# Performance work log

Hardware: AMD Instinct MI355X
Metric: run time of the kernel (lower is better)

## Reference

```python
import jax, jax.numpy as jnp
import numpy as np

B = 4096          # players (batch)
DEG = 64          # asteroids per player
A = B * DEG       # total asteroids
E = A             # one edge per asteroid (asteroid -> its player)
PD, AD, ED = 5, 3, 7
HID = 64
HEADS = 4
OUT = HID         # GATv2Conv out_channels (concat=False -> mean over heads)
L = 2             # num_layers
NEG_SLOPE = 0.2
LN_EPS = 1e-5


def setup_inputs() -> dict:
    key = jax.random.key(0)
    ks = jax.random.split(key, 20)
    f = jnp.float32
    inp = {}
    inp["player_feat"] = jax.random.normal(ks[0], (B, PD), f)
    inp["asteroid_feat"] = jax.random.normal(ks[1], (A, AD), f)
    src = jnp.arange(E, dtype=jnp.int32)
    dst = src // DEG                      # player batch index per edge
    inp["edge_index"] = jnp.stack([src, dst])  # [2, E] int32
    inp["edge_attr"] = jax.random.normal(ks[2], (E, ED), f)
    sc = 0.1
    # input projections
    inp["Wp"] = jax.random.normal(ks[3], (PD, HID), f) * sc
    inp["bp"] = jnp.zeros((HID,), f)
    inp["Wa"] = jax.random.normal(ks[4], (AD, HID), f) * sc
    inp["ba"] = jnp.zeros((HID,), f)
    # per-layer GATv2 params (stacked over L)
    inp["Wl"] = jax.random.normal(ks[5], (L, HID, HEADS * OUT), f) * sc
    inp["bl"] = jnp.zeros((L, HEADS * OUT), f)
    inp["Wr"] = jax.random.normal(ks[6], (L, HID, HEADS * OUT), f) * sc
    inp["br"] = jnp.zeros((L, HEADS * OUT), f)
    inp["We"] = jax.random.normal(ks[7], (L, ED, HEADS * OUT), f) * sc
    inp["att"] = jax.random.normal(ks[8], (L, HEADS, OUT), f) * sc
    inp["bias"] = jnp.zeros((L, OUT), f)
    inp["ln_g"] = jnp.ones((L, HID), f)
    inp["ln_b"] = jnp.zeros((L, HID), f)
    return inp


def _layer_norm(x, g, b):
    mu = jnp.mean(x, axis=-1, keepdims=True)
    var = jnp.mean(jnp.square(x - mu), axis=-1, keepdims=True)
    return (x - mu) * jax.lax.rsqrt(var + LN_EPS) * g + b


def _gatv2(x, src, dst, edge_attr, Wl, bl, Wr, br, We, att, bias, n_nodes):
    # x: [N, HID]; src/dst: [E]; PyG GATv2Conv, add_self_loops=False, concat=False
    xl = (x @ Wl + bl).reshape(-1, HEADS, OUT)   # source transform
    xr = (x @ Wr + br).reshape(-1, HEADS, OUT)   # target transform
    ea = (edge_attr @ We).reshape(-1, HEADS, OUT)
    e = xl[src] + xr[dst] + ea                   # [E, H, O]
    e = jnp.where(e >= 0, e, NEG_SLOPE * e)      # LeakyReLU(0.2)
    logits = jnp.einsum('eho,ho->eh', e, att)    # [E, H]
    # segment softmax over incoming edges of each target node
    m = jax.ops.segment_max(logits, dst, num_segments=n_nodes)
    al = jnp.exp(logits - m[dst])
    den = jax.ops.segment_sum(al, dst, num_segments=n_nodes)
    alpha = al / den[dst]                        # [E, H]
    msg = alpha[:, :, None] * xl[src]            # [E, H, O]
    out = jax.ops.segment_sum(msg, dst, num_segments=n_nodes)  # [N, H, O]
    return jnp.mean(out, axis=1) + bias          # concat=False -> head mean


def reference(player_feat, asteroid_feat, edge_index, edge_attr,
              Wp, bp, Wa, ba, Wl, bl, Wr, br, We, att, bias, ln_g, ln_b):
    batch = player_feat.shape[0]
    h_p = jax.nn.relu(player_feat @ Wp + bp)
    h_a = jax.nn.relu(asteroid_feat @ Wa + ba)
    x = jnp.concatenate([h_p, h_a], axis=0)      # [N, HID]
    n_nodes = x.shape[0]
    src = edge_index[0] + batch                  # asteroid local -> global idx
    dst = edge_index[1]
    for i in range(L):
        x_new = _gatv2(x, src, dst, edge_attr, Wl[i], bl[i], Wr[i], br[i],
                       We[i], att[i], bias[i], n_nodes)
        x = _layer_norm(x + jax.nn.relu(x_new), ln_g[i], ln_b[i])
    return x[:batch]
```

## Files before the change

### kernel.cpp

```cpp
#include <hip/hip_runtime.h>


typedef __bf16 bf16x8 __attribute__((ext_vector_type(8)));
typedef float  f32x4  __attribute__((ext_vector_type(4)));

union FragU { unsigned short u[8]; bf16x8 v; };

__device__ __forceinline__ float bf2f(unsigned short u) {
    union { unsigned int i; float f; } v; v.i = ((unsigned int)u) << 16; return v.f;
}
__device__ __forceinline__ unsigned short f2bf(float f) {
    union { float f; unsigned int i; } v; v.f = f;
    unsigned int r = v.i + 0x7fffu + ((v.i >> 16) & 1u);
    return (unsigned short)(r >> 16);
}

#define NEG_SLOPE 0.2f
#define LN_EPS 1e-5f
#define XS 88

struct Smem {
    __align__(16) unsigned short xa[64 * XS];
    float xp[64];
    float xr[256];
    float outp[256];
    float afs[192];
    float rbs[64], gs[64], bs[64];
};

__global__ __launch_bounds__(256) void prep_weights(
    const float* __restrict__ Wl, const float* __restrict__ We,
    unsigned short* __restrict__ wlf, unsigned short* __restrict__ wef)
{
    int i = blockIdx.x * 256 + threadIdx.x;
    {
        int jj = i & 7, t = (i >> 3) & 255, frag = (i >> 11) & 7, layer = (i >> 14) & 1;
        int nt = frag >> 1, ko = frag & 1;
        int c = (t >> 6) * 64 + nt * 16 + (t & 15);
        int kb = ko * 32 + ((t >> 4) & 3) * 8;
        wlf[i] = f2bf(Wl[layer * 16384 + (kb + jj) * 256 + c]);
    }
    if (i < 16384) {
        int jj = i & 7, t = (i >> 3) & 255, nt = (i >> 11) & 3, layer = (i >> 13) & 1;
        int q = (t >> 4) & 3;
        int c = (t >> 6) * 64 + nt * 16 + (t & 15);
        wef[i] = (q == 0 && jj < 7) ? f2bf(We[layer * 1792 + jj * 256 + c])
                                    : (unsigned short)0;
    }
}

template <bool WS>
__global__ __launch_bounds__(256) void gnn_main(
    const float* __restrict__ pf, const float* __restrict__ af,
    const float* __restrict__ eat, const float* __restrict__ Wp,
    const float* __restrict__ bp, const float* __restrict__ Wa,
    const float* __restrict__ ba, const float* __restrict__ Wl,
    const float* __restrict__ bl, const float* __restrict__ Wr,
    const float* __restrict__ br, const float* __restrict__ We,
    const float* __restrict__ att, const float* __restrict__ bias,
    const float* __restrict__ lng, const float* __restrict__ lnb,
    const unsigned short* __restrict__ wlf, const unsigned short* __restrict__ wef,
    float* __restrict__ out)
{
    __shared__ Smem sm;
    const int p = blockIdx.x, t = threadIdx.x;
    const int w = t >> 6, l = t & 63, q = l >> 4, m = l & 15;
    const int cbase = w * 64;

    if (t < 192) sm.afs[t] = af[p * 192 + t];
    if (t < 64) {
        sm.rbs[t] = fmaxf(bias[t], 0.f);
        sm.gs[t] = lng[t];
        sm.bs[t] = lnb[t];
        float acc = bp[t];
        #pragma unroll
        for (int d = 0; d < 5; ++d) acc += pf[p * 5 + d] * Wp[d * 64 + t];
        sm.xp[t] = fmaxf(acc, 0.f);
    }
    __syncthreads();
    {
        const int k = t & 63;
        float wa0 = Wa[k], wa1 = Wa[64 + k], wa2 = Wa[128 + k], bak = ba[k];
        #pragma unroll
        for (int rep = 0; rep < 16; ++rep) {
            int j = rep * 4 + (t >> 6);
            float acc = bak + sm.afs[j * 3] * wa0 + sm.afs[j * 3 + 1] * wa1
                      + sm.afs[j * 3 + 2] * wa2;
            sm.xa[j * XS + k] = f2bf(fmaxf(acc, 0.f));
        }
    }
    #pragma unroll
    for (int idx = t; idx < 512; idx += 256) {
        int j = idx >> 3, d = idx & 7;
        sm.xa[j * XS + 64 + d] = (d < 7) ? f2bf(eat[(p * 64 + j) * 7 + d])
                                         : (unsigned short)0;
    }
    __syncthreads();

    f32x4 accT[16];

    for (int layer = 0; layer < 2; ++layer) {
        {
            float acc = br[layer * 256 + t];
            const float* Wri = Wr + layer * 16384 + t;
            #pragma unroll 16
            for (int k = 0; k < 64; ++k) acc += sm.xp[k] * Wri[k * 256];
            sm.xr[t] = acc;
        }
        __syncthreads();

        FragU bfr[8];
        bf16x8 ebf[4];
        if constexpr (WS) {
            #pragma unroll
            for (int f = 0; f < 8; ++f)
                bfr[f].v = *reinterpret_cast<const bf16x8*>(&wlf[((layer * 8 + f) * 256 + t) * 8]);
            #pragma unroll
            for (int nt = 0; nt < 4; ++nt)
                ebf[nt] = *reinterpret_cast<const bf16x8*>(&wef[((layer * 4 + nt) * 256 + t) * 8]);
        } else {
            const float* Wli = Wl + layer * 16384;
            #pragma unroll
            for (int nt = 0; nt < 4; ++nt) {
                int c = cbase + nt * 16 + m;
                #pragma unroll
                for (int ko = 0; ko < 2; ++ko) {
                    int kb = ko * 32 + q * 8;
                    #pragma unroll
                    for (int jj = 0; jj < 8; ++jj)
                        bfr[nt * 2 + ko].u[jj] = f2bf(Wli[(kb + jj) * 256 + c]);
                }
                FragU e;
                #pragma unroll
                for (int jj = 0; jj < 8; ++jj)
                    e.u[jj] = (q == 0 && jj < 7) ? f2bf(We[layer * 1792 + jj * 256 + c])
                                                 : (unsigned short)0;
                ebf[nt] = e.v;
            }
        }
        float blc[4], xrc[4], aoc[4];
        #pragma unroll
        for (int nt = 0; nt < 4; ++nt) {
            int c = cbase + nt * 16 + m;
            blc[nt] = bl[layer * 256 + c];
            aoc[nt] = att[layer * 256 + c];
            xrc[nt] = sm.xr[c];
        }

        float lp[16];
        #pragma unroll
        for (int i = 0; i < 16; ++i) lp[i] = 0.f;

        #pragma unroll
        for (int mt = 0; mt < 4; ++mt) {
            const int row = mt * 16 + m;
            bf16x8 a0 = *reinterpret_cast<const bf16x8*>(&sm.xa[row * XS + q * 8]);
            bf16x8 a1 = *reinterpret_cast<const bf16x8*>(&sm.xa[row * XS + 32 + q * 8]);
            bf16x8 a2 = *reinterpret_cast<const bf16x8*>(&sm.xa[row * XS + 64]);
            #pragma unroll
            for (int nt = 0; nt < 4; ++nt) {
                f32x4 c1 = { blc[nt], blc[nt], blc[nt], blc[nt] };
                c1 = __builtin_amdgcn_mfma_f32_16x16x32_bf16(a0, bfr[nt * 2 + 0].v, c1, 0, 0, 0);
                c1 = __builtin_amdgcn_mfma_f32_16x16x32_bf16(a1, bfr[nt * 2 + 1].v, c1, 0, 0, 0);
                accT[mt * 4 + nt] = c1;
                f32x4 c2 = { xrc[nt], xrc[nt], xrc[nt], xrc[nt] };
                c2 = __builtin_amdgcn_mfma_f32_16x16x32_bf16(a2, ebf[nt], c2, 0, 0, 0);
                #pragma unroll
                for (int r = 0; r < 4; ++r) {
                    float ev = c1[r] + c2[r];
                    ev = (ev >= 0.f) ? ev : NEG_SLOPE * ev;
                    lp[mt * 4 + r] += ev * aoc[nt];
                }
            }
        }

        #pragma unroll
        for (int i = 0; i < 16; ++i) {
            float v = lp[i];
            v += __shfl_xor(v, 1, 64);
            v += __shfl_xor(v, 2, 64);
            v += __shfl_xor(v, 4, 64);
            v += __shfl_xor(v, 8, 64);
            lp[i] = v;
        }
        float mx = lp[0];
        #pragma unroll
        for (int i = 1; i < 16; ++i) mx = fmaxf(mx, lp[i]);
        mx = fmaxf(mx, __shfl_xor(mx, 16, 64));
        mx = fmaxf(mx, __shfl_xor(mx, 32, 64));
        float den = 0.f;
        #pragma unroll
        for (int i = 0; i < 16; ++i) { lp[i] = __expf(lp[i] - mx); den += lp[i]; }
        den += __shfl_xor(den, 16, 64);
        den += __shfl_xor(den, 32, 64);
        const float rden = 1.f / den;

        #pragma unroll
        for (int nt = 0; nt < 4; ++nt) {
            float s = 0.f;
            #pragma unroll
            for (int mt = 0; mt < 4; ++mt) {
                f32x4 c = accT[mt * 4 + nt];
                #pragma unroll
                for (int r = 0; r < 4; ++r) s += lp[mt * 4 + r] * c[r];
            }
            s *= rden;
            s += __shfl_xor(s, 16, 64);
            s += __shfl_xor(s, 32, 64);
            if (q == 0) sm.outp[cbase + nt * 16 + m] = s;
        }
        __syncthreads();

        if (layer == 0) {
            const int j = t >> 2, part = t & 3;
            unsigned short* rowp = &sm.xa[j * XS + part * 16];
            FragU A0, A1;
            A0.v = *reinterpret_cast<const bf16x8*>(rowp);
            A1.v = *reinterpret_cast<const bf16x8*>(rowp + 8);
            float v[16], sum = 0.f, sq = 0.f;
            #pragma unroll
            for (int i = 0; i < 16; ++i) {
                unsigned short us = (i < 8) ? A0.u[i] : A1.u[i - 8];
                float x = bf2f(us) + sm.rbs[part * 16 + i];
                v[i] = x; sum += x; sq += x * x;
            }
            sum += __shfl_xor(sum, 1, 64); sq += __shfl_xor(sq, 1, 64);
            sum += __shfl_xor(sum, 2, 64); sq += __shfl_xor(sq, 2, 64);
            float mu = sum * (1.f / 64.f);
            float var = sq * (1.f / 64.f) - mu * mu;
            float rs = rsqrtf(var + LN_EPS);
            FragU O0, O1;
            #pragma unroll
            for (int i = 0; i < 16; ++i) {
                int col = part * 16 + i;
                float y = (v[i] - mu) * rs * sm.gs[col] + sm.bs[col];
                unsigned short ub = f2bf(y);
                if (i < 8) O0.u[i] = ub; else O1.u[i - 8] = ub;
            }
            *reinterpret_cast<bf16x8*>(rowp) = O0.v;
            *reinterpret_cast<bf16x8*>(rowp + 8) = O1.v;
        }
        if (t < 64) {
            float xnew = 0.25f * (sm.outp[t] + sm.outp[64 + t] + sm.outp[128 + t] + sm.outp[192 + t])
                       + bias[layer * 64 + t];
            float v = sm.xp[t] + fmaxf(xnew, 0.f);
            float sum = v, sq = v * v;
            #pragma unroll
            for (int msk = 1; msk <= 32; msk <<= 1) {
                sum += __shfl_xor(sum, msk, 64);
                sq  += __shfl_xor(sq,  msk, 64);
            }
            float mu = sum * (1.f / 64.f);
            float var = sq * (1.f / 64.f) - mu * mu;
            float y = (v - mu) * rsqrtf(var + LN_EPS) * lng[layer * 64 + t]
                    + lnb[layer * 64 + t];
            sm.xp[t] = y;
        }
        __syncthreads();
    }

    if (t < 64) out[p * 64 + t] = sm.xp[t];
}

extern "C" void kernel_launch(void* const* d_in, const int* in_sizes, int n_in,
                              void* d_out, int out_size, void* d_ws, size_t ws_size,
                              hipStream_t stream) {
    const float* pf   = (const float*)d_in[0];
    const float* af   = (const float*)d_in[1];
    const float* eat  = (const float*)d_in[3];
    const float* Wp   = (const float*)d_in[4];
    const float* bp   = (const float*)d_in[5];
    const float* Wa   = (const float*)d_in[6];
    const float* ba   = (const float*)d_in[7];
    const float* Wl   = (const float*)d_in[8];
    const float* bl   = (const float*)d_in[9];
    const float* Wr   = (const float*)d_in[10];
    const float* br   = (const float*)d_in[11];
    const float* We   = (const float*)d_in[12];
    const float* att  = (const float*)d_in[13];
    const float* bias = (const float*)d_in[14];
    const float* lng  = (const float*)d_in[15];
    const float* lnb  = (const float*)d_in[16];
    float* out = (float*)d_out;

    const int B = in_sizes[0] / 5;
    unsigned short* wlf = (unsigned short*)d_ws;
    unsigned short* wef = wlf + 32768;
    const size_t need = 98304;

    if (ws_size >= need) {
        prep_weights<<<dim3(128), dim3(256), 0, stream>>>(Wl, We, wlf, wef);
        gnn_main<true><<<dim3(B), dim3(256), 0, stream>>>(
            pf, af, eat, Wp, bp, Wa, ba, Wl, bl, Wr, br, We, att, bias, lng, lnb,
            wlf, wef, out);
    } else {
        gnn_main<false><<<dim3(B), dim3(256), 0, stream>>>(
            pf, af, eat, Wp, bp, Wa, ba, Wl, bl, Wr, br, We, att, bias, lng, lnb,
            wlf, wef, out);
    }
}
```

Measured before the change: 203.2 us.

## Compute Wr projection with MFMA and restructure softmax through shared memory

The per-player target transform (xp @ Wr) now runs as bf16 MFMA using Wr fragments pre-converted by the prep kernel. This replaces a 64-step scalar fp32 loop of strided global loads per thread. The per-row attention logits are transposed through padded shared memory and reduced per lane, replacing the many cross-lane shuffle reductions. Biases and attention vectors are also staged in LDS, and bf16 conversion now uses the native cast. The cost is lower precision on the xp/Wr path, a larger LDS footprint and extra block barriers.

```diff
diff --git a/kernel.cpp b/kernel.cpp
--- a/kernel.cpp
+++ b/kernel.cpp
@@ -10,42 +10,45 @@
     union { unsigned int i; float f; } v; v.i = ((unsigned int)u) << 16; return v.f;
 }
 __device__ __forceinline__ unsigned short f2bf(float f) {
-    union { float f; unsigned int i; } v; v.f = f;
-    unsigned int r = v.i + 0x7fffu + ((v.i >> 16) & 1u);
-    return (unsigned short)(r >> 16);
+    union { __bf16 b; unsigned short u; } x; x.b = (__bf16)f; return x.u;
 }
 
 #define NEG_SLOPE 0.2f
 #define LN_EPS 1e-5f
 #define XS 88
+#define LPS 17
 
 struct Smem {
     __align__(16) unsigned short xa[64 * XS];
+    __align__(16) unsigned short xpb[64];
+    float lpb[4 * 64 * LPS];
+    float alf[256];
+    float outp[256];
     float xp[64];
-    float xr[256];
-    float outp[256];
     float afs[192];
     float rbs[64], gs[64], bs[64];
+    float sbl[256], satt[256], sbr[256];
 };
 
 __global__ __launch_bounds__(256) void prep_weights(
-    const float* __restrict__ Wl, const float* __restrict__ We,
-    unsigned short* __restrict__ wlf, unsigned short* __restrict__ wef)
+    const float* __restrict__ Wl, const float* __restrict__ Wr,
+    const float* __restrict__ We,
+    unsigned short* __restrict__ wlf, unsigned short* __restrict__ wrf,
+    unsigned short* __restrict__ wef)
 {
     int i = blockIdx.x * 256 + threadIdx.x;
-    {
-        int jj = i & 7, t = (i >> 3) & 255, frag = (i >> 11) & 7, layer = (i >> 14) & 1;
-        int nt = frag >> 1, ko = frag & 1;
-        int c = (t >> 6) * 64 + nt * 16 + (t & 15);
-        int kb = ko * 32 + ((t >> 4) & 3) * 8;
-        wlf[i] = f2bf(Wl[layer * 16384 + (kb + jj) * 256 + c]);
-    }
+    int jj = i & 7, t = (i >> 3) & 255, frag = (i >> 11) & 7, layer = (i >> 14) & 1;
+    int nt = frag >> 1, ko = frag & 1;
+    int c = (t >> 6) * 64 + nt * 16 + (t & 15);
+    int kb = ko * 32 + ((t >> 4) & 3) * 8;
+    wlf[i] = f2bf(Wl[layer * 16384 + (kb + jj) * 256 + c]);
+    wrf[i] = f2bf(Wr[layer * 16384 + (kb + jj) * 256 + c]);
     if (i < 16384) {
-        int jj = i & 7, t = (i >> 3) & 255, nt = (i >> 11) & 3, layer = (i >> 13) & 1;
-        int q = (t >> 4) & 3;
-        int c = (t >> 6) * 64 + nt * 16 + (t & 15);
-        wef[i] = (q == 0 && jj < 7) ? f2bf(We[layer * 1792 + jj * 256 + c])
-                                    : (unsigned short)0;
+        int j2 = i & 7, t2 = (i >> 3) & 255, n2 = (i >> 11) & 3, l2 = (i >> 13) & 1;
+        int q2 = (t2 >> 4) & 3;
+        int c2 = (t2 >> 6) * 64 + n2 * 16 + (t2 & 15);
+        wef[i] = (q2 == 0 && j2 < 7) ? f2bf(We[l2 * 1792 + j2 * 256 + c2])
+                                     : (unsigned short)0;
     }
 }
 
@@ -59,8 +62,8 @@
     const float* __restrict__ br, const float* __restrict__ We,
     const float* __restrict__ att, const float* __restrict__ bias,
     const float* __restrict__ lng, const float* __restrict__ lnb,
-    const unsigned short* __restrict__ wlf, const unsigned short* __restrict__ wef,
-    float* __restrict__ out)
+    const unsigned short* __restrict__ wlf, const unsigned short* __restrict__ wrf,
+    const unsigned short* __restrict__ wef, float* __restrict__ out)
 {
     __shared__ Smem sm;
     const int p = blockIdx.x, t = threadIdx.x;
@@ -75,7 +78,9 @@
         float acc = bp[t];
         #pragma unroll
         for (int d = 0; d < 5; ++d) acc += pf[p * 5 + d] * Wp[d * 64 + t];
-        sm.xp[t] = fmaxf(acc, 0.f);
+        float xp0 = fmaxf(acc, 0.f);
+        sm.xp[t] = xp0;
+        sm.xpb[t] = f2bf(xp0);
     }
     __syncthreads();
     {
@@ -95,19 +100,41 @@
         sm.xa[j * XS + 64 + d] = (d < 7) ? f2bf(eat[(p * 64 + j) * 7 + d])
                                          : (unsigned short)0;
     }
-    __syncthreads();
 
     f32x4 accT[16];
 
     for (int layer = 0; layer < 2; ++layer) {
+        sm.sbl[t]  = bl[layer * 256 + t];
+        sm.satt[t] = att[layer * 256 + t];
+        sm.sbr[t]  = br[layer * 256 + t];
+        __syncthreads();
+
+        float xrc[4];
         {
-            float acc = br[layer * 256 + t];
-            const float* Wri = Wr + layer * 16384 + t;
-            #pragma unroll 16
-            for (int k = 0; k < 64; ++k) acc += sm.xp[k] * Wri[k * 256];
-            sm.xr[t] = acc;
-        }
-        __syncthreads();
+            FragU xf0, xf1;
+            xf0.v = *reinterpret_cast<const bf16x8*>(&sm.xpb[q * 8]);
+            xf1.v = *reinterpret_cast<const bf16x8*>(&sm.xpb[32 + q * 8]);
+            #pragma unroll
+            for (int nt = 0; nt < 4; ++nt) {
+                int c = cbase + nt * 16 + m;
+                FragU r0, r1;
+                if constexpr (WS) {
+                    r0.v = *reinterpret_cast<const bf16x8*>(&wrf[((layer * 8 + nt * 2 + 0) * 256 + t) * 8]);
+                    r1.v = *reinterpret_cast<const bf16x8*>(&wrf[((layer * 8 + nt * 2 + 1) * 256 + t) * 8]);
+                } else {
+                    #pragma unroll
+                    for (int jj = 0; jj < 8; ++jj) {
+                        r0.u[jj] = f2bf(Wr[layer * 16384 + (q * 8 + jj) * 256 + c]);
+                        r1.u[jj] = f2bf(Wr[layer * 16384 + (32 + q * 8 + jj) * 256 + c]);
+                    }
+                }
+                float sb = sm.sbr[c];
+                f32x4 cx = { sb, sb, sb, sb };
+                cx = __builtin_amdgcn_mfma_f32_16x16x32_bf16(xf0.v, r0.v, cx, 0, 0, 0);
+                cx = __builtin_amdgcn_mfma_f32_16x16x32_bf16(xf1.v, r1.v, cx, 0, 0, 0);
+                xrc[nt] = cx[0];
+            }
+        }
 
         FragU bfr[8];
         bf16x8 ebf[4];
@@ -138,13 +165,12 @@
                 ebf[nt] = e.v;
             }
         }
-        float blc[4], xrc[4], aoc[4];
+        float blc[4], aoc[4];
         #pragma unroll
         for (int nt = 0; nt < 4; ++nt) {
             int c = cbase + nt * 16 + m;
-            blc[nt] = bl[layer * 256 + c];
-            aoc[nt] = att[layer * 256 + c];
-            xrc[nt] = sm.xr[c];
+            blc[nt] = sm.sbl[c];
+            aoc[nt] = sm.satt[c];
         }
 
         float lp[16];
@@ -168,46 +194,54 @@
                 #pragma unroll
                 for (int r = 0; r < 4; ++r) {
                     float ev = c1[r] + c2[r];
-                    ev = (ev >= 0.f) ? ev : NEG_SLOPE * ev;
+                    ev = fmaxf(ev, NEG_SLOPE * ev);
                     lp[mt * 4 + r] += ev * aoc[nt];
                 }
             }
         }
 
-        #pragma unroll
-        for (int i = 0; i < 16; ++i) {
-            float v = lp[i];
-            v += __shfl_xor(v, 1, 64);
-            v += __shfl_xor(v, 2, 64);
-            v += __shfl_xor(v, 4, 64);
-            v += __shfl_xor(v, 8, 64);
-            lp[i] = v;
-        }
-        float mx = lp[0];
-        #pragma unroll
-        for (int i = 1; i < 16; ++i) mx = fmaxf(mx, lp[i]);
-        mx = fmaxf(mx, __shfl_xor(mx, 16, 64));
-        mx = fmaxf(mx, __shfl_xor(mx, 32, 64));
-        float den = 0.f;
-        #pragma unroll
-        for (int i = 0; i < 16; ++i) { lp[i] = __expf(lp[i] - mx); den += lp[i]; }
-        den += __shfl_xor(den, 16, 64);
-        den += __shfl_xor(den, 32, 64);
-        const float rden = 1.f / den;
-
-        #pragma unroll
-        for (int nt = 0; nt < 4; ++nt) {
-            float s = 0.f;
-            #pragma unroll
-            for (int mt = 0; mt < 4; ++mt) {
-                f32x4 c = accT[mt * 4 + nt];
-                #pragma unroll
-                for (int r = 0; r < 4; ++r) s += lp[mt * 4 + r] * c[r];
-            }
-            s *= rden;
-            s += __shfl_xor(s, 16, 64);
-            s += __shfl_xor(s, 32, 64);
-            if (q == 0) sm.outp[cbase + nt * 16 + m] = s;
+        {
+            float* lpw = &sm.lpb[w * 64 * LPS];
+            #pragma unroll
+            for (int mt = 0; mt < 4; ++mt)
+                #pragma unroll
+                for (int r = 0; r < 4; ++r)
+                    lpw[(mt * 16 + q * 4 + r) * LPS + m] = lp[mt * 4 + r];
+        }
+        __syncthreads();
+        {
+            const float* lpw = &sm.lpb[w * 64 * LPS];
+            float lg = 0.f;
+            #pragma unroll
+            for (int mm = 0; mm < 16; ++mm) lg += lpw[l * LPS + mm];
+            float mx = lg;
+            #pragma unroll
+            for (int msk = 1; msk <= 32; msk <<= 1) mx = fmaxf(mx, __shfl_xor(mx, msk, 64));
+            float al = __expf(lg - mx);
+            float den = al;
+            #pragma unroll
+            for (int msk = 1; msk <= 32; msk <<= 1) den += __shfl_xor(den, msk, 64);
+            sm.alf[w * 64 + l] = al / den;
+        }
+        __syncthreads();
+
+        {
+            const float* alw = &sm.alf[w * 64];
+            float al16[16];
+            #pragma unroll
+            for (int mt = 0; mt < 4; ++mt)
+                #pragma unroll
+                for (int r = 0; r < 4; ++r)
+                    al16[mt * 4 + r] = alw[mt * 16 + q * 4 + r];
+            #pragma unroll
+            for (int nt = 0; nt < 4; ++nt) {
+                float s = 0.f;
+                #pragma unroll
+                for (int i = 0; i < 16; ++i) s += al16[i] * accT[(i >> 2) * 4 + nt][i & 3];
+                s += __shfl_xor(s, 16, 64);
+                s += __shfl_xor(s, 32, 64);
+                if (q == 0) sm.outp[cbase + nt * 16 + m] = s;
+            }
         }
         __syncthreads();
 
@@ -233,8 +267,7 @@
             #pragma unroll
             for (int i = 0; i < 16; ++i) {
                 int col = part * 16 + i;
-                float y = (v[i] - mu) * rs * sm.gs[col] + sm.bs[col];
-                unsigned short ub = f2bf(y);
+                unsigned short ub = f2bf((v[i] - mu) * rs * sm.gs[col] + sm.bs[col]);
                 if (i < 8) O0.u[i] = ub; else O1.u[i - 8] = ub;
             }
             *reinterpret_cast<bf16x8*>(rowp) = O0.v;
@@ -255,6 +288,7 @@
             float y = (v - mu) * rsqrtf(var + LN_EPS) * lng[layer * 64 + t]
                     + lnb[layer * 64 + t];
             sm.xp[t] = y;
+            sm.xpb[t] = f2bf(y);
         }
         __syncthreads();
     }
@@ -285,17 +319,18 @@
 
     const int B = in_sizes[0] / 5;
     unsigned short* wlf = (unsigned short*)d_ws;
-    unsigned short* wef = wlf + 32768;
-    const size_t need = 98304;
+    unsigned short* wrf = wlf + 32768;
+    unsigned short* wef = wrf + 32768;
+    const size_t need = (32768 + 32768 + 16384) * sizeof(unsigned short);
 
     if (ws_size >= need) {
-        prep_weights<<<dim3(128), dim3(256), 0, stream>>>(Wl, We, wlf, wef);
+        prep_weights<<<dim3(128), dim3(256), 0, stream>>>(Wl, Wr, We, wlf, wrf, wef);
         gnn_main<true><<<dim3(B), dim3(256), 0, stream>>>(
             pf, af, eat, Wp, bp, Wa, ba, Wl, bl, Wr, br, We, att, bias, lng, lnb,
-            wlf, wef, out);
+            wlf, wrf, wef, out);
     } else {
         gnn_main<false><<<dim3(B), dim3(256), 0, stream>>>(
             pf, af, eat, Wp, bp, Wa, ba, Wl, bl, Wr, br, We, att, bias, lng, lnb,
-            wlf, wef, out);
-    }
-}
+            wlf, wrf, wef, out);
+    }
+}
```

New measurement: 181.7 us. 1.12x faster.
